# Kernel optimization log

Hardware: AMD Instinct MI355X
Metric: run time of the kernel (lower is better)

The kernel has to match this reference:

```python
import jax, jax.numpy as jnp
import numpy as np

LEVELS = 256  # graylevels; init kwarg levels=256


def setup_inputs() -> dict:
    key = jax.random.key(0)
    # intensities in [0,1); quantized to uint8-like levels inside reference
    x = jax.random.uniform(key, (32, 1, 512, 512), dtype=jnp.float32)
    return {"x": x}


def _glcm_props(x):
    # quantize to integer gray levels (mirrors .astype(np.uint8))
    img = jnp.clip((x[:, 0] * LEVELS).astype(jnp.int32), 0, LEVELS - 1)  # [B,H,W]
    # distance=1, angle=0 -> horizontal neighbor pairs (r,c)->(r,c+1)
    left = img[:, :, :-1]
    right = img[:, :, 1:]
    bins = (left * LEVELS + right).reshape(img.shape[0], -1)  # [B, H*(W-1)]

    def hist_one(b):
        return jnp.zeros(LEVELS * LEVELS, jnp.float32).at[b].add(1.0)

    P = jax.vmap(hist_one)(bins).reshape(-1, LEVELS, LEVELS)  # [B,L,L]
    P = P + jnp.swapaxes(P, 1, 2)            # symmetric=True
    P = P / jnp.sum(P, axis=(1, 2), keepdims=True)  # normed=True

    i = jnp.arange(LEVELS, dtype=jnp.float32)[:, None]  # row index
    j = jnp.arange(LEVELS, dtype=jnp.float32)[None, :]  # col index
    diff = i - j

    contrast = jnp.sum(P * diff**2, axis=(1, 2))
    dissimilarity = jnp.sum(P * jnp.abs(diff), axis=(1, 2))
    homogeneity = jnp.sum(P / (1.0 + diff**2), axis=(1, 2))
    energy = jnp.sqrt(jnp.sum(P**2, axis=(1, 2)))  # sqrt(ASM)

    mu_i = jnp.sum(P * i, axis=(1, 2))
    mu_j = jnp.sum(P * j, axis=(1, 2))
    var_i = jnp.sum(P * (i - mu_i[:, None, None]) ** 2, axis=(1, 2))
    var_j = jnp.sum(P * (j - mu_j[:, None, None]) ** 2, axis=(1, 2))
    std_i = jnp.sqrt(var_i)
    std_j = jnp.sqrt(var_j)
    cov = jnp.sum(P * (i - mu_i[:, None, None]) * (j - mu_j[:, None, None]), axis=(1, 2))
    eps = 1e-15
    denom = jnp.where(std_i * std_j < eps, 1.0, std_i * std_j)
    correlation = jnp.where(std_i * std_j < eps, 1.0, cov / denom)

    # concat order: contrast, dissimilarity, homogeneity, energy, correlation
    return jnp.stack([contrast, dissimilarity, homogeneity, energy, correlation], axis=1)  # [B,5]


def reference(x):
    return _glcm_props(x)
```

## Files before the change

### kernel.cpp

```cpp
#include <hip/hip_runtime.h>

constexpr int NIMG   = 32;
constexpr int W      = 512;
constexpr int S      = 8;
constexpr int ROWS   = W / S;
constexpr int HW_C   = 32896;
constexpr int WORDS_C = HW_C / 2;
constexpr int U4_C   = WORDS_C / 4;
constexpr int K2     = 16;
constexpr int U4_PC  = U4_C / K2;
constexpr float SUMQ = 2.0f * 511.0f * 512.0f;

__device__ __forceinline__ void tri_add(unsigned int* sh, int a, int b) {
    int d = (a > b) ? (a - b) : (b - a);
    int m = (a < b) ? a : b;
    int h = ((d * (513 - d)) >> 1) + m;
    atomicAdd(&sh[h >> 1], 1u << ((h & 1) << 4));
}

__device__ __forceinline__ int quant(float v) {
    int q = (int)(v * 256.0f);
    return min(255, max(0, q));
}

__device__ __forceinline__ float wave_red(float v) {
#pragma unroll
    for (int off = 32; off; off >>= 1) v += __shfl_down(v, off);
    return v;
}

__global__ void __launch_bounds__(1024)
glcm_hist(const float* __restrict__ x, uint4* __restrict__ hist,
          unsigned int* __restrict__ tickets) {
    __shared__ unsigned int sh[WORDS_C];
    const int t   = threadIdx.x;
    const int bid = blockIdx.x;

    if (bid < NIMG && t == 0) tickets[bid] = 0;

    uint4* sh4 = reinterpret_cast<uint4*>(sh);
    for (int g = t; g < U4_C; g += 1024) sh4[g] = uint4{0u, 0u, 0u, 0u};
    __syncthreads();

    const float* __restrict__ xb = x + (size_t)bid * ROWS * W;
    const int nf4 = ROWS * (W / 4);

    for (int f = t; f < nf4; f += 1024) {
        float4 v = reinterpret_cast<const float4*>(xb)[f];
        int b0 = quant(v.x);
        int b1 = quant(v.y);
        int b2 = quant(v.z);
        int b3 = quant(v.w);
        tri_add(sh, b0, b1);
        tri_add(sh, b1, b2);
        tri_add(sh, b2, b3);
        if ((f & (W / 4 - 1)) != (W / 4 - 1)) {
            int b4 = quant(xb[f * 4 + 4]);
            tri_add(sh, b3, b4);
        }
    }
    __syncthreads();

    uint4* __restrict__ hb = hist + (size_t)bid * U4_C;
    for (int g = t; g < U4_C; g += 1024) hb[g] = sh4[g];
}

__global__ void __launch_bounds__(256)
glcm_feat(const uint4* __restrict__ hist, float* __restrict__ part,
          unsigned int* __restrict__ tickets, float* __restrict__ out) {
    const int img   = blockIdx.x >> 4;
    const int chunk = blockIdx.x & 15;
    const uint4* __restrict__ hb = hist + (size_t)img * S * U4_C;

    float s_con = 0.f, s_dis = 0.f, s_hom = 0.f;
    float s_i = 0.f, s_ii = 0.f, s_ij = 0.f, s_q2 = 0.f;

    for (int g = threadIdx.x; g < U4_PC; g += 256) {
        const int g_abs = chunk * U4_PC + g;

        unsigned int c0 = 0, c1 = 0, c2 = 0, c3 = 0, c4 = 0, c5 = 0, c6 = 0, c7 = 0;
#pragma unroll
        for (int s = 0; s < S; ++s) {
            uint4 v = hb[(size_t)s * U4_C + g_abs];
            c0 += v.x & 0xFFFFu;  c1 += v.x >> 16;
            c2 += v.y & 0xFFFFu;  c3 += v.y >> 16;
            c4 += v.z & 0xFFFFu;  c5 += v.z >> 16;
            c6 += v.w & 0xFFFFu;  c7 += v.w >> 16;
        }
        unsigned int cc[8] = {c0, c1, c2, c3, c4, c5, c6, c7};

        const int h0 = g_abs << 3;
        int d = (int)((513.0f - sqrtf((float)(263169 - 8 * h0))) * 0.5f);
        while ((d * (513 - d)) / 2 > h0) --d;
        while (((d + 1) * (512 - d)) / 2 <= h0) ++d;
        int i = h0 - (d * (513 - d)) / 2;

        const float wq = (g_abs < 32) ? 2.0f : 1.0f;
#pragma unroll
        for (int k = 0; k < 8; ++k) {
            float fc = (float)cc[k];
            float fd = (float)d;
            float fi = (float)i;
            float fj = fi + fd;
            s_con += fc * fd * fd;
            s_dis += fc * fd;
            s_hom += fc / (1.0f + fd * fd);
            s_i   += fc * (fi + fj);
            s_ii  += fc * (fi * fi + fj * fj);
            s_ij  += fc * fi * fj;
            s_q2  += wq * fc * fc;
            if (++i == 256 - d) { ++d; i = 0; }
        }
    }

    float vals[7] = {s_con, s_dis, s_hom, s_i, s_ii, s_ij, s_q2};
    __shared__ float red[4][7];
    const int lane = threadIdx.x & 63;
    const int wv   = threadIdx.x >> 6;
#pragma unroll
    for (int q = 0; q < 7; ++q) {
        float v = wave_red(vals[q]);
        if (lane == 0) red[wv][q] = v;
    }
    __syncthreads();

    if (threadIdx.x == 0) {
        float* p = part + (size_t)(img * K2 + chunk) * 8;
#pragma unroll
        for (int q = 0; q < 7; ++q)
            p[q] = red[0][q] + red[1][q] + red[2][q] + red[3][q];

        __threadfence();
        unsigned int prev = atomicAdd(&tickets[img], 1u);
        if (prev == K2 - 1) {
            __threadfence();
            float m[7] = {0.f, 0.f, 0.f, 0.f, 0.f, 0.f, 0.f};
            for (int c = 0; c < K2; ++c) {
                const float* q = part + (size_t)(img * K2 + c) * 8;
#pragma unroll
                for (int k = 0; k < 7; ++k) m[k] += q[k];
            }
            const float inv = 1.0f / SUMQ;
            float contrast = 2.0f * m[0] * inv;
            float dissim   = 2.0f * m[1] * inv;
            float homog    = 2.0f * m[2] * inv;
            float mu       = m[3] * inv;
            float var      = m[4] * inv - mu * mu;
            float cov      = 2.0f * m[5] * inv - mu * mu;
            float energy   = sqrtf(2.0f * m[6]) * inv;
            float corr     = (var < 1e-15f) ? 1.0f : (cov / var);

            out[img * 5 + 0] = contrast;
            out[img * 5 + 1] = dissim;
            out[img * 5 + 2] = homog;
            out[img * 5 + 3] = energy;
            out[img * 5 + 4] = corr;
        }
    }
}

extern "C" void kernel_launch(void* const* d_in, const int* in_sizes, int n_in,
                              void* d_out, int out_size, void* d_ws, size_t ws_size,
                              hipStream_t stream) {
    const float* x = (const float*)d_in[0];
    float* out = (float*)d_out;

    uint4* hist = (uint4*)d_ws;
    float* part = (float*)((char*)d_ws + (size_t)NIMG * S * U4_C * sizeof(uint4));
    unsigned int* tickets = (unsigned int*)(part + (size_t)NIMG * K2 * 8);

    glcm_hist<<<NIMG * S, 1024, 0, stream>>>(x, hist, tickets);
    glcm_feat<<<NIMG * K2, 256, 0, stream>>>(hist, part, tickets, out);
}
```

Baseline: 33.19 us.

## Double histogram slices, shuffle neighbor bins, and drop per-call ticket reset

Splits each image into 16 row slices instead of 8, giving the histogram kernel twice as many blocks with half the rows each. The feature kernel must then sum 16 partial histograms per bin, so workspace size and read traffic double. Each lane now gets the right-neighbour pixel's bin from the next lane with a shuffle, and only the last lane does an extra global load. The ticket counter is no longer reset each call; instead the last block is detected with a modulo-16 check on release/acquire atomics, and the hash index uses __mul24. The ticket scheme relies on the counter starting at a multiple of 16.

After: 58.44 us. +76.1%, slower.

```diff
diff --git a/kernel.cpp b/kernel.cpp
--- a/kernel.cpp
+++ b/kernel.cpp
@@ -1,20 +1,20 @@
 #include <hip/hip_runtime.h>
 
-constexpr int NIMG   = 32;
-constexpr int W      = 512;
-constexpr int S      = 8;
-constexpr int ROWS   = W / S;
-constexpr int HW_C   = 32896;
+constexpr int NIMG    = 32;
+constexpr int W       = 512;
+constexpr int S       = 16;
+constexpr int ROWS    = W / S;
+constexpr int HW_C    = 32896;
 constexpr int WORDS_C = HW_C / 2;
-constexpr int U4_C   = WORDS_C / 4;
-constexpr int K2     = 16;
-constexpr int U4_PC  = U4_C / K2;
-constexpr float SUMQ = 2.0f * 511.0f * 512.0f;
+constexpr int U4_C    = WORDS_C / 4;
+constexpr int K2C     = 16;
+constexpr int U4_PC   = U4_C / K2C;
+constexpr float SUMQ  = 2.0f * 511.0f * 512.0f;
 
 __device__ __forceinline__ void tri_add(unsigned int* sh, int a, int b) {
     int d = (a > b) ? (a - b) : (b - a);
     int m = (a < b) ? a : b;
-    int h = ((d * (513 - d)) >> 1) + m;
+    int h = (__mul24(d, 513 - d) >> 1) + m;
     atomicAdd(&sh[h >> 1], 1u << ((h & 1) << 4));
 }
 
@@ -30,13 +30,11 @@
 }
 
 __global__ void __launch_bounds__(1024)
-glcm_hist(const float* __restrict__ x, uint4* __restrict__ hist,
-          unsigned int* __restrict__ tickets) {
+glcm_hist(const float* __restrict__ x, uint4* __restrict__ hist) {
     __shared__ unsigned int sh[WORDS_C];
-    const int t   = threadIdx.x;
-    const int bid = blockIdx.x;
-
-    if (bid < NIMG && t == 0) tickets[bid] = 0;
+    const int t    = threadIdx.x;
+    const int bid  = blockIdx.x;
+    const int lane = t & 63;
 
     uint4* sh4 = reinterpret_cast<uint4*>(sh);
     for (int g = t; g < U4_C; g += 1024) sh4[g] = uint4{0u, 0u, 0u, 0u};
@@ -51,11 +49,12 @@
         int b1 = quant(v.y);
         int b2 = quant(v.z);
         int b3 = quant(v.w);
+        int nb0 = __shfl_down(b0, 1);
         tri_add(sh, b0, b1);
         tri_add(sh, b1, b2);
         tri_add(sh, b2, b3);
         if ((f & (W / 4 - 1)) != (W / 4 - 1)) {
-            int b4 = quant(xb[f * 4 + 4]);
+            int b4 = (lane == 63) ? quant(xb[f * 4 + 4]) : nb0;
             tri_add(sh, b3, b4);
         }
     }
@@ -125,20 +124,23 @@
     __syncthreads();
 
     if (threadIdx.x == 0) {
-        float* p = part + (size_t)(img * K2 + chunk) * 8;
+        float* p = part + (size_t)(img * K2C + chunk) * 8;
 #pragma unroll
         for (int q = 0; q < 7; ++q)
-            p[q] = red[0][q] + red[1][q] + red[2][q] + red[3][q];
+            __hip_atomic_store(&p[q], red[0][q] + red[1][q] + red[2][q] + red[3][q],
+                               __ATOMIC_RELEASE, __HIP_MEMORY_SCOPE_AGENT);
 
-        __threadfence();
-        unsigned int prev = atomicAdd(&tickets[img], 1u);
-        if (prev == K2 - 1) {
-            __threadfence();
+        unsigned int prev = __hip_atomic_fetch_add(&tickets[img], 1u,
+                                                   __ATOMIC_ACQ_REL,
+                                                   __HIP_MEMORY_SCOPE_AGENT);
+        if ((prev & 15u) == 15u) {
             float m[7] = {0.f, 0.f, 0.f, 0.f, 0.f, 0.f, 0.f};
-            for (int c = 0; c < K2; ++c) {
-                const float* q = part + (size_t)(img * K2 + c) * 8;
+            for (int c = 0; c < K2C; ++c) {
+                const float* q = part + (size_t)(img * K2C + c) * 8;
 #pragma unroll
-                for (int k = 0; k < 7; ++k) m[k] += q[k];
+                for (int k = 0; k < 7; ++k)
+                    m[k] += __hip_atomic_load(&q[k], __ATOMIC_RELAXED,
+                                              __HIP_MEMORY_SCOPE_AGENT);
             }
             const float inv = 1.0f / SUMQ;
             float contrast = 2.0f * m[0] * inv;
@@ -167,8 +169,8 @@
 
     uint4* hist = (uint4*)d_ws;
     float* part = (float*)((char*)d_ws + (size_t)NIMG * S * U4_C * sizeof(uint4));
-    unsigned int* tickets = (unsigned int*)(part + (size_t)NIMG * K2 * 8);
+    unsigned int* tickets = (unsigned int*)(part + (size_t)NIMG * K2C * 8);
 
-    glcm_hist<<<NIMG * S, 1024, 0, stream>>>(x, hist, tickets);
-    glcm_feat<<<NIMG * K2, 256, 0, stream>>>(hist, part, tickets, out);
+    glcm_hist<<<NIMG * S, 1024, 0, stream>>>(x, hist);
+    glcm_feat<<<NIMG * K2C, 256, 0, stream>>>(hist, part, tickets, out);
 }
```
